# Kernel tuning notes

Measured on AMD Instinct MI355X. Metric: run time of the kernel, lower is better.

Reference implementation:

```python
import jax, jax.numpy as jnp
import numpy as np

NUM_HEADS = 4

def setup_inputs() -> dict:
    key = jax.random.key(0)
    ks = jax.random.split(key, 5)
    B, T, F, C = 2, 128, 256, 256
    # weights scaled ~1/sqrt(C) so softmax is not saturated
    s = 1.0 / np.sqrt(C)
    return {
        "x": jax.random.normal(ks[0], (B, T, F, C), jnp.float32),
        "w_in": jax.random.normal(ks[1], (3 * C, C), jnp.float32) * s,
        "b_in": jax.random.normal(ks[2], (3 * C,), jnp.float32) * 0.01,
        "w_out": jax.random.normal(ks[3], (C, C), jnp.float32) * s,
        "b_out": jax.random.normal(ks[4], (C,), jnp.float32) * 0.01,
        "band": 16,
    }

def reference(x, w_in, b_in, w_out, b_out, band):
    B, T, F, C = x.shape
    H = NUM_HEADS
    D = C // H
    x2 = x.reshape(B * T, F, C)  # attention over frequency, independent per (B,T)
    qkv = x2 @ w_in.T + b_in  # [BT, F, 3C]
    q, k, v = jnp.split(qkv, 3, axis=-1)
    def heads(t):
        return t.reshape(B * T, F, H, D).transpose(0, 2, 1, 3)  # [BT, H, F, D]
    q, k, v = heads(q), heads(k), heads(v)
    scores = jnp.einsum('bhid,bhjd->bhij', q, k) / jnp.sqrt(jnp.asarray(D, x.dtype))
    i = jnp.arange(F)[:, None]
    j = jnp.arange(F)[None, :]
    keep = jnp.abs(i - j) <= band  # banded locality mask [F, F]
    scores = jnp.where(keep, scores, -jnp.inf)
    attn = jax.nn.softmax(scores, axis=-1)
    out = jnp.einsum('bhij,bhjd->bhid', attn, v)  # [BT, H, F, D]
    out = out.transpose(0, 2, 1, 3).reshape(B * T, F, C)
    y = out @ w_out.T + b_out
    return y.reshape(B, T, F, C)
```

## Files before the change

### kernel.cpp

```cpp
#include <hip/hip_runtime.h>
#include <hip/hip_bf16.h>
#include <cstdint>

typedef unsigned int u32;
typedef __attribute__((ext_vector_type(8))) __bf16 bf16x8;
typedef __attribute__((ext_vector_type(4))) float f32x4;
typedef __attribute__((ext_vector_type(2))) _Float16 half2_t;
typedef __attribute__((ext_vector_type(4))) _Float16 half4;
typedef __attribute__((ext_vector_type(2))) __fp16 fp16x2;

#define BT_N 256
#define F_N 256
#define C_N 256
#define H_N 4
#define D_N 64
#define TC_N 768
#define M_N (BT_N * F_N)
#define VT_ST 268

__device__ __forceinline__ ushort f2bf(float f) {
  u32 u = __float_as_uint(f);
  u32 r = (u + 0x7fffu + ((u >> 16) & 1u)) >> 16;
  return (ushort)r;
}

__device__ __forceinline__ u32 pkbf(float a, float b) {
  return (u32)f2bf(a) | ((u32)f2bf(b) << 16);
}

__device__ __forceinline__ void gload_lds16(const ushort* g, ushort* l) {
  __builtin_amdgcn_global_load_lds(
      (const __attribute__((address_space(1))) u32*)g,
      (__attribute__((address_space(3))) u32*)l, 16, 0, 0);
}

#define WAITV(N) asm volatile("s_waitcnt vmcnt(" #N ")" ::: "memory")
#define BAR_IN  { __builtin_amdgcn_s_barrier(); \
                  asm volatile("" ::: "memory"); \
                  __builtin_amdgcn_sched_barrier(0); }
#define BAR_OUT { __builtin_amdgcn_sched_barrier(0); \
                  asm volatile("" ::: "memory"); \
                  __builtin_amdgcn_s_barrier(); }

__global__ __launch_bounds__(256) void cvt2_f32_bf16_k(
    const float* __restrict__ s0, ushort* __restrict__ d0, int n0,
    const float* __restrict__ s1, ushort* __restrict__ d1, int n1) {
  int idx = blockIdx.x * 256 + threadIdx.x;
  int stride = gridDim.x * 256;
  for (int i = idx; i < n0 + n1; i += stride) {
    const float4* s = (i < n0) ? ((const float4*)s0 + i) : ((const float4*)s1 + (i - n0));
    ushort* d = (i < n0) ? (d0 + (size_t)i * 4) : (d1 + (size_t)(i - n0) * 4);
    float4 v = *s;
    *(uint2*)d = make_uint2(pkbf(v.x, v.y), pkbf(v.z, v.w));
  }
}

__global__ __launch_bounds__(256) void gemm_qkv(
    const float* __restrict__ x, const ushort* __restrict__ wb,
    const float* __restrict__ bias, _Float16* __restrict__ qkv, int nwg8) {
  __shared__ ushort Bs[2][128 * 64];

  const int tid = threadIdx.x;
  const int lane = tid & 63;
  const int wid = tid >> 6;
  const int wr = wid >> 1, wc = wid & 1;
  const int l15 = lane & 15, g = lane >> 4;
  const int b = blockIdx.x;
  const int bid = (b & 7) * nwg8 + (b >> 3);
  const int rowBase = bid * 64;

  bf16x8 af[2][8];
#pragma unroll
  for (int i2 = 0; i2 < 2; ++i2) {
    const float* xr = x + (size_t)(rowBase + wr * 32 + i2 * 16 + l15) * 256 + g * 8;
#pragma unroll
    for (int ks = 0; ks < 8; ++ks) {
      float4 f0 = *(const float4*)(xr + ks * 32);
      float4 f1 = *(const float4*)(xr + ks * 32 + 4);
      uint4 pk = make_uint4(pkbf(f0.x, f0.y), pkbf(f0.z, f0.w),
                            pkbf(f1.x, f1.y), pkbf(f1.z, f1.w));
      af[i2][ks] = __builtin_bit_cast(bf16x8, pk);
    }
  }

  const int sr = tid >> 3;
  const int sc = tid & 7;
#define STAGE_B(buf, nt, kt)                                                  \
  {                                                                           \
    ushort* B_ = Bs[buf];                                                     \
    _Pragma("unroll") for (int p = 0; p < 4; ++p) {                           \
      int r = p * 32 + sr;                                                    \
      const ushort* gb = wb + (size_t)((nt) * 128 + r) * 256 + (kt) * 64 +    \
                         ((sc ^ (r & 7)) << 3);                               \
      gload_lds16(gb, B_ + (size_t)(p * 256 + tid) * 8);                      \
    }                                                                         \
  }

  f32x4 acc[2][4] = {};
  STAGE_B(0, 0, 0);

#pragma unroll
  for (int nt = 0; nt < 6; ++nt) {
#pragma unroll
    for (int kt = 0; kt < 4; ++kt) {
      const int s = nt * 4 + kt;
      if (s < 23) {
        const int nt2 = (s + 1) >> 2, kt2 = (s + 1) & 3;
        STAGE_B((s + 1) & 1, nt2, kt2);
        WAITV(4);
      } else {
        WAITV(0);
      }
      BAR_IN;
      const ushort* B_ = Bs[s & 1];
#pragma unroll
      for (int kk = 0; kk < 2; ++kk) {
        bf16x8 bfr[4];
#pragma unroll
        for (int j2 = 0; j2 < 4; ++j2) {
          int row = wc * 64 + j2 * 16 + l15;
          bfr[j2] = *(const bf16x8*)(B_ + row * 64 + (((kk * 4 + g) ^ (l15 & 7)) * 8));
        }
#pragma unroll
        for (int i2 = 0; i2 < 2; ++i2)
#pragma unroll
          for (int j2 = 0; j2 < 4; ++j2)
            acc[i2][j2] = __builtin_amdgcn_mfma_f32_16x16x32_bf16(
                bfr[j2], af[i2][kt * 2 + kk], acc[i2][j2], 0, 0, 0);
      }
      if (kt == 3) {
#pragma unroll
        for (int j2 = 0; j2 < 4; ++j2) {
          int col = nt * 128 + wc * 64 + j2 * 16 + g * 4;
          float4 bv = *(const float4*)(bias + col);
#pragma unroll
          for (int i2 = 0; i2 < 2; ++i2) {
            int row = rowBase + wr * 32 + i2 * 16 + l15;
            fp16x2 lo = __builtin_amdgcn_cvt_pkrtz(acc[i2][j2][0] + bv.x,
                                                   acc[i2][j2][1] + bv.y);
            fp16x2 hi = __builtin_amdgcn_cvt_pkrtz(acc[i2][j2][2] + bv.z,
                                                   acc[i2][j2][3] + bv.w);
            *(uint2*)(qkv + (size_t)row * 768 + col) =
                make_uint2(__builtin_bit_cast(u32, lo), __builtin_bit_cast(u32, hi));
            acc[i2][j2] = f32x4{0.f, 0.f, 0.f, 0.f};
          }
        }
      }
      BAR_OUT;
    }
  }
#undef STAGE_B
}

template <typename OutT>
__global__ __launch_bounds__(256, 2) void gemm_bt(
    const ushort* __restrict__ Ap, const ushort* __restrict__ Bp,
    const float* __restrict__ bias, OutT* __restrict__ Cp,
    int N, int NTN, int nwg8) {
  constexpr bool F32OUT = (sizeof(OutT) == 4);
  constexpr int SMEM_BYTES = F32OUT ? 67584 : 65536;
  __shared__ char smem[SMEM_BYTES];
  ushort* smemH = (ushort*)smem;

  const int tid = threadIdx.x;
  const int lane = tid & 63;
  const int wid = tid >> 6;
  const int wr = wid >> 1, wc = wid & 1;
  const int l15 = lane & 15, l4 = lane >> 4;
  const int b = blockIdx.x;
  const int bid = (b & 7) * nwg8 + (b >> 3);
  const int tm = bid / NTN;
  const int tn = bid - tm * NTN;
  const int rowBase = tm * 128, colBase = tn * 128;

  f32x4 acc[4][4] = {};

  const int ar = (tid >> 3);
  const int c8 = tid & 7;
  const int akk = ((c8 ^ (ar & 7)) << 3);
  const ushort* gB = Bp + (size_t)(colBase + ar) * 256 + akk;
  const ushort* gAh = Ap + (size_t)(rowBase + ar) * 256 + akk;

#define STAGE_AB(buf, k0)                                                     \
  {                                                                           \
    ushort* As_ = smemH + (buf) * 8192;                                       \
    ushort* Bs_ = smemH + 16384 + (buf) * 8192;                               \
    _Pragma("unroll") for (int c = 0; c < 4; ++c) {                           \
      gload_lds16(gAh + (size_t)(c * 32) * 256 + (k0),                        \
                  As_ + (size_t)(c * 256 + (wid << 6)) * 8);                  \
      gload_lds16(gB + (size_t)(c * 32) * 256 + (k0),                         \
                  Bs_ + (size_t)(c * 256 + (wid << 6)) * 8);                  \
    }                                                                         \
  }

  STAGE_AB(0, 0);

  int cur = 0;
#pragma unroll
  for (int t = 0; t < 4; ++t) {
    if (t < 3) {
      STAGE_AB(cur ^ 1, (t + 1) * 64);
      WAITV(8);
    } else {
      WAITV(0);
    }
    BAR_IN;
    const ushort* As_ = smemH + cur * 8192;
    const ushort* Bs_ = smemH + 16384 + cur * 8192;
#pragma unroll
    for (int kk = 0; kk < 2; ++kk) {
      bf16x8 af[4];
      bf16x8 bfr[4];
#pragma unroll
      for (int i2 = 0; i2 < 4; ++i2) {
        int row = wr * 64 + i2 * 16 + l15;
        af[i2] = *(const bf16x8*)(As_ + row * 64 + (((kk * 4 + l4) ^ (l15 & 7)) * 8));
      }
#pragma unroll
      for (int j2 = 0; j2 < 4; ++j2) {
        int row = wc * 64 + j2 * 16 + l15;
        bfr[j2] = *(const bf16x8*)(Bs_ + row * 64 + (((kk * 4 + l4) ^ (l15 & 7)) * 8));
      }
#pragma unroll
      for (int i2 = 0; i2 < 4; ++i2)
#pragma unroll
        for (int j2 = 0; j2 < 4; ++j2)
          acc[i2][j2] = __builtin_amdgcn_mfma_f32_16x16x32_bf16(
              af[i2], bfr[j2], acc[i2][j2], 0, 0, 0);
    }
    BAR_OUT;
    cur ^= 1;
  }
#undef STAGE_AB

  __syncthreads();
  if constexpr (F32OUT) {
    float* eb = (float*)smem;
#pragma unroll
    for (int j2 = 0; j2 < 4; ++j2) {
      float bv = bias[colBase + wc * 64 + j2 * 16 + l15];
#pragma unroll
      for (int i2 = 0; i2 < 4; ++i2)
#pragma unroll
        for (int r = 0; r < 4; ++r)
          eb[(wr * 64 + i2 * 16 + l4 * 4 + r) * 132 + wc * 64 + j2 * 16 + l15] =
              acc[i2][j2][r] + bv;
    }
    __syncthreads();
#pragma unroll
    for (int i = 0; i < 32; ++i) {
      int row = wid * 32 + i;
      uint2 d = *(const uint2*)((const u32*)eb + row * 132 + lane * 2);
      *(uint2*)((float*)Cp + (size_t)(rowBase + row) * N + colBase + lane * 2) = d;
    }
  } else {
    ushort* eb = smemH;
#pragma unroll
    for (int j2 = 0; j2 < 4; ++j2) {
      float bv = bias[colBase + wc * 64 + j2 * 16 + l15];
#pragma unroll
      for (int i2 = 0; i2 < 4; ++i2)
#pragma unroll
        for (int r = 0; r < 4; ++r) {
          _Float16 h = (_Float16)(acc[i2][j2][r] + bv);
          eb[(wr * 64 + i2 * 16 + l4 * 4 + r) * 136 + wc * 64 + j2 * 16 + l15] =
              __builtin_bit_cast(ushort, h);
        }
    }
    __syncthreads();
#pragma unroll
    for (int i = 0; i < 16; ++i) {
      int row = wid * 32 + 2 * i + (lane >> 5);
      int hl = lane & 31;
      uint2 d = *(const uint2*)(eb + row * 136 + hl * 4);
      *(uint2*)((_Float16*)Cp + (size_t)(rowBase + row) * N + colBase + hl * 4) = d;
    }
  }
}

__global__ __launch_bounds__(256) void attn_mfma(
    const _Float16* __restrict__ qkv, ushort* __restrict__ aout) {
  __shared__ ushort smem[18432 + 64 * VT_ST];
  const int tid = threadIdx.x;
  const int bt = blockIdx.x >> 2;
  const int h = blockIdx.x & 3;
  const _Float16* base = qkv + (size_t)bt * 256 * 768 + h * 64;
  ushort* klds = smem;
  ushort* vlds = smem + 18432;

  {
    const int r0 = tid >> 3, c8 = tid & 7;
#pragma unroll
    for (int p = 0; p < 8; ++p) {
      int j = p * 32 + r0;
      const uint4 k4 = *(const uint4*)(base + (size_t)j * 768 + 256 + c8 * 8);
      *(uint4*)(klds + j * 72 + c8 * 8) = k4;
      const uint4 v4 = *(const uint4*)(base + (size_t)j * 768 + 512 + c8 * 8);
      const ushort* vh = (const ushort*)&v4;
      ushort* vtp = vlds + (c8 * 8) * VT_ST + j;
#pragma unroll
      for (int i = 0; i < 8; ++i) vtp[i * VT_ST] = vh[i];
    }
  }

  const int w = tid >> 6, lane = tid & 63;
  const int l15 = lane & 15, g = lane >> 4, g4 = g * 4;

  uint2 qf0[4], qf1[4], qf2[4], qf3[4];
  {
    const uint2* q0 = (const uint2*)(base + (size_t)(w * 64 + 0 * 16 + l15) * 768 + g4);
    const uint2* q1 = (const uint2*)(base + (size_t)(w * 64 + 1 * 16 + l15) * 768 + g4);
    const uint2* q2 = (const uint2*)(base + (size_t)(w * 64 + 2 * 16 + l15) * 768 + g4);
    const uint2* q3 = (const uint2*)(base + (size_t)(w * 64 + 3 * 16 + l15) * 768 + g4);
#pragma unroll
    for (int ks = 0; ks < 4; ++ks) {
      qf0[ks] = q0[ks * 4]; qf1[ks] = q1[ks * 4];
      qf2[ks] = q2[ks * 4]; qf3[ks] = q3[ks * 4];
    }
  }

  u32 bb = 0;
#pragma unroll
  for (int jt = 0; jt < 3; ++jt)
#pragma unroll
    for (int r = 0; r < 4; ++r) {
      int d = 16 * jt + g4 + r - 16 - l15;
      if (d >= -16 && d <= 16) bb |= 1u << (jt * 4 + r);
    }

  __syncthreads();

  const float SC = 0.18033688f;

#pragma unroll
  for (int rt = 0; rt < 4; ++rt) {
    const int R0 = w * 64 + rt * 16;
    const int Jc = R0 - 16;
    const uint2* qf = (rt == 0) ? qf0 : (rt == 1) ? qf1 : (rt == 2) ? qf2 : qf3;

    f32x4 st[3] = {};
#pragma unroll
    for (int jt = 0; jt < 3; ++jt) {
      int krow = Jc + 16 * jt + l15;
      krow = krow < 0 ? 0 : (krow > 255 ? 255 : krow);
      const ushort* kp = klds + krow * 72 + g4;
#pragma unroll
      for (int ks = 0; ks < 4; ++ks) {
        uint2 kf = *(const uint2*)(kp + ks * 16);
        st[jt] = __builtin_amdgcn_mfma_f32_16x16x16f16(
            __builtin_bit_cast(half4, kf), __builtin_bit_cast(half4, qf[ks]),
            st[jt], 0, 0, 0);
      }
    }

    float l_acc = 0.f;
    float pp[3][4];
#pragma unroll
    for (int jt = 0; jt < 3; ++jt)
#pragma unroll
      for (int r = 0; r < 4; ++r) {
        int jg = Jc + 16 * jt + g4 + r;
        bool keep = (((bb >> (jt * 4 + r)) & 1u) != 0) && (jg >= 0) && (jg < 256);
        float pv = keep ? __builtin_amdgcn_exp2f(st[jt][r] * SC) : 0.f;
        pp[jt][r] = pv;
        l_acc += pv;
      }
    l_acc += __shfl_xor(l_acc, 16, 64);
    l_acc += __shfl_xor(l_acc, 32, 64);
    const float inv = 1.f / l_acc;

    uint2 pf[3];
#pragma unroll
    for (int jt = 0; jt < 3; ++jt) {
      fp16x2 a = __builtin_amdgcn_cvt_pkrtz(pp[jt][0] * inv, pp[jt][1] * inv);
      fp16x2 c = __builtin_amdgcn_cvt_pkrtz(pp[jt][2] * inv, pp[jt][3] * inv);
      pf[jt].x = __builtin_bit_cast(u32, a);
      pf[jt].y = __builtin_bit_cast(u32, c);
    }

    f32x4 ot[4] = {};
#pragma unroll
    for (int kt = 0; kt < 3; ++kt) {
      int jb = Jc + 16 * kt + g4;
      jb = jb < 0 ? 0 : (jb > 252 ? 252 : jb);
#pragma unroll
      for (int mt = 0; mt < 4; ++mt) {
        uint2 vfr = *(const uint2*)(vlds + (16 * mt + l15) * VT_ST + jb);
        ot[mt] = __builtin_amdgcn_mfma_f32_16x16x16f16(
            __builtin_bit_cast(half4, vfr), __builtin_bit_cast(half4, pf[kt]),
            ot[mt], 0, 0, 0);
      }
    }

    ushort* orow = aout + (size_t)(bt * 256 + R0 + l15) * 256 + h * 64 + g4;
#pragma unroll
    for (int mt = 0; mt < 4; ++mt) {
      u32 lo = (u32)f2bf(ot[mt][0]) | ((u32)f2bf(ot[mt][1]) << 16);
      u32 hi = (u32)f2bf(ot[mt][2]) | ((u32)f2bf(ot[mt][3]) << 16);
      *(uint2*)(orow + mt * 16) = make_uint2(lo, hi);
    }
  }
}

extern "C" void kernel_launch(void* const* d_in, const int* in_sizes, int n_in,
                              void* d_out, int out_size, void* d_ws, size_t ws_size,
                              hipStream_t stream) {
  const float* x = (const float*)d_in[0];
  const float* w_in = (const float*)d_in[1];
  const float* b_in = (const float*)d_in[2];
  const float* w_out = (const float*)d_in[3];
  const float* b_out = (const float*)d_in[4];
  float* y = (float*)d_out;

  char* ws = (char*)d_ws;
  const size_t qkv_bytes = (size_t)M_N * TC_N * 2;
  _Float16* qkv = (_Float16*)ws;
  ushort* attn = (ushort*)(ws + qkv_bytes);
  ushort* winb = attn + (size_t)M_N * C_N;
  ushort* woutb = winb + TC_N * C_N;

  cvt2_f32_bf16_k<<<256, 256, 0, stream>>>(w_in, winb, TC_N * C_N / 4,
                                           w_out, woutb, C_N * C_N / 4);

  gemm_qkv<<<M_N / 64, 256, 0, stream>>>(x, winb, b_in, qkv, (M_N / 64) / 8);

  attn_mfma<<<BT_N * H_N, 256, 0, stream>>>(qkv, attn);

  gemm_bt<float><<<(M_N / 128) * (C_N / 128), 256, 0, stream>>>(
      attn, woutb, b_out, y, C_N, C_N / 128, (M_N / 128) * (C_N / 128) / 8);
}
```

Baseline: 111.4 us.

## Restructure QKV GEMM into 128x128 tiles with fp32 A staged via LDS

Replaces the QKV projection kernel, which held one 64-row A block in registers and swept all 768 columns. The new kernel uses 128x128 output tiles with double-buffered LDS for both operands. A is loaded as fp32, converted to bf16 in registers, and written to swizzled LDS, while B uses direct global-to-LDS loads. The epilogue stages fp16 results through LDS so stores are coalesced. The intent is better MFMA utilization and store efficiency, at the cost of re-reading the fp32 input once per column tile.

```diff
diff --git a/kernel.cpp b/kernel.cpp
--- a/kernel.cpp
+++ b/kernel.cpp
@@ -35,6 +35,9 @@
 }
 
 #define WAITV(N) asm volatile("s_waitcnt vmcnt(" #N ")" ::: "memory")
+#define BARX { asm volatile("s_waitcnt lgkmcnt(0)" ::: "memory"); \
+               __builtin_amdgcn_s_barrier(); \
+               __builtin_amdgcn_sched_barrier(0); }
 #define BAR_IN  { __builtin_amdgcn_s_barrier(); \
                   asm volatile("" ::: "memory"); \
                   __builtin_amdgcn_sched_barrier(0); }
@@ -55,111 +58,11 @@
   }
 }
 
-__global__ __launch_bounds__(256) void gemm_qkv(
-    const float* __restrict__ x, const ushort* __restrict__ wb,
-    const float* __restrict__ bias, _Float16* __restrict__ qkv, int nwg8) {
-  __shared__ ushort Bs[2][128 * 64];
-
-  const int tid = threadIdx.x;
-  const int lane = tid & 63;
-  const int wid = tid >> 6;
-  const int wr = wid >> 1, wc = wid & 1;
-  const int l15 = lane & 15, g = lane >> 4;
-  const int b = blockIdx.x;
-  const int bid = (b & 7) * nwg8 + (b >> 3);
-  const int rowBase = bid * 64;
-
-  bf16x8 af[2][8];
-#pragma unroll
-  for (int i2 = 0; i2 < 2; ++i2) {
-    const float* xr = x + (size_t)(rowBase + wr * 32 + i2 * 16 + l15) * 256 + g * 8;
-#pragma unroll
-    for (int ks = 0; ks < 8; ++ks) {
-      float4 f0 = *(const float4*)(xr + ks * 32);
-      float4 f1 = *(const float4*)(xr + ks * 32 + 4);
-      uint4 pk = make_uint4(pkbf(f0.x, f0.y), pkbf(f0.z, f0.w),
-                            pkbf(f1.x, f1.y), pkbf(f1.z, f1.w));
-      af[i2][ks] = __builtin_bit_cast(bf16x8, pk);
-    }
-  }
-
-  const int sr = tid >> 3;
-  const int sc = tid & 7;
-#define STAGE_B(buf, nt, kt)                                                  \
-  {                                                                           \
-    ushort* B_ = Bs[buf];                                                     \
-    _Pragma("unroll") for (int p = 0; p < 4; ++p) {                           \
-      int r = p * 32 + sr;                                                    \
-      const ushort* gb = wb + (size_t)((nt) * 128 + r) * 256 + (kt) * 64 +    \
-                         ((sc ^ (r & 7)) << 3);                               \
-      gload_lds16(gb, B_ + (size_t)(p * 256 + tid) * 8);                      \
-    }                                                                         \
-  }
-
-  f32x4 acc[2][4] = {};
-  STAGE_B(0, 0, 0);
-
-#pragma unroll
-  for (int nt = 0; nt < 6; ++nt) {
-#pragma unroll
-    for (int kt = 0; kt < 4; ++kt) {
-      const int s = nt * 4 + kt;
-      if (s < 23) {
-        const int nt2 = (s + 1) >> 2, kt2 = (s + 1) & 3;
-        STAGE_B((s + 1) & 1, nt2, kt2);
-        WAITV(4);
-      } else {
-        WAITV(0);
-      }
-      BAR_IN;
-      const ushort* B_ = Bs[s & 1];
-#pragma unroll
-      for (int kk = 0; kk < 2; ++kk) {
-        bf16x8 bfr[4];
-#pragma unroll
-        for (int j2 = 0; j2 < 4; ++j2) {
-          int row = wc * 64 + j2 * 16 + l15;
-          bfr[j2] = *(const bf16x8*)(B_ + row * 64 + (((kk * 4 + g) ^ (l15 & 7)) * 8));
-        }
-#pragma unroll
-        for (int i2 = 0; i2 < 2; ++i2)
-#pragma unroll
-          for (int j2 = 0; j2 < 4; ++j2)
-            acc[i2][j2] = __builtin_amdgcn_mfma_f32_16x16x32_bf16(
-                bfr[j2], af[i2][kt * 2 + kk], acc[i2][j2], 0, 0, 0);
-      }
-      if (kt == 3) {
-#pragma unroll
-        for (int j2 = 0; j2 < 4; ++j2) {
-          int col = nt * 128 + wc * 64 + j2 * 16 + g * 4;
-          float4 bv = *(const float4*)(bias + col);
-#pragma unroll
-          for (int i2 = 0; i2 < 2; ++i2) {
-            int row = rowBase + wr * 32 + i2 * 16 + l15;
-            fp16x2 lo = __builtin_amdgcn_cvt_pkrtz(acc[i2][j2][0] + bv.x,
-                                                   acc[i2][j2][1] + bv.y);
-            fp16x2 hi = __builtin_amdgcn_cvt_pkrtz(acc[i2][j2][2] + bv.z,
-                                                   acc[i2][j2][3] + bv.w);
-            *(uint2*)(qkv + (size_t)row * 768 + col) =
-                make_uint2(__builtin_bit_cast(u32, lo), __builtin_bit_cast(u32, hi));
-            acc[i2][j2] = f32x4{0.f, 0.f, 0.f, 0.f};
-          }
-        }
-      }
-      BAR_OUT;
-    }
-  }
-#undef STAGE_B
-}
-
-template <typename OutT>
-__global__ __launch_bounds__(256, 2) void gemm_bt(
-    const ushort* __restrict__ Ap, const ushort* __restrict__ Bp,
-    const float* __restrict__ bias, OutT* __restrict__ Cp,
-    int N, int NTN, int nwg8) {
-  constexpr bool F32OUT = (sizeof(OutT) == 4);
-  constexpr int SMEM_BYTES = F32OUT ? 67584 : 65536;
-  __shared__ char smem[SMEM_BYTES];
+__global__ __launch_bounds__(256, 2) void gemm_qkv_f32(
+    const float* __restrict__ x, const ushort* __restrict__ Bp,
+    const float* __restrict__ bias, _Float16* __restrict__ Cp,
+    int NTN, int nwg8) {
+  __shared__ char smem[65536];
   ushort* smemH = (ushort*)smem;
 
   const int tid = threadIdx.x;
@@ -179,6 +82,132 @@
   const int c8 = tid & 7;
   const int akk = ((c8 ^ (ar & 7)) << 3);
   const ushort* gB = Bp + (size_t)(colBase + ar) * 256 + akk;
+  const float* gA = x + (size_t)(rowBase + ar) * 256 + akk;
+
+  float4 rA[2][4][2];
+
+#define LOAD_AF(rb, k0)                                                       \
+  {                                                                           \
+    _Pragma("unroll") for (int c = 0; c < 4; ++c) {                           \
+      const float* ga = gA + (size_t)(c * 32) * 256 + (k0);                   \
+      rA[rb][c][0] = *(const float4*)ga;                                      \
+      rA[rb][c][1] = *(const float4*)(ga + 4);                                \
+    }                                                                         \
+  }
+#define WRITE_AF(lb, rb)                                                      \
+  {                                                                           \
+    ushort* As_ = smemH + (lb) * 8192;                                        \
+    _Pragma("unroll") for (int c = 0; c < 4; ++c) {                           \
+      uint4 pk = make_uint4(pkbf(rA[rb][c][0].x, rA[rb][c][0].y),             \
+                            pkbf(rA[rb][c][0].z, rA[rb][c][0].w),             \
+                            pkbf(rA[rb][c][1].x, rA[rb][c][1].y),             \
+                            pkbf(rA[rb][c][1].z, rA[rb][c][1].w));            \
+      *(uint4*)(As_ + (ar + 32 * c) * 64 + c8 * 8) = pk;                      \
+    }                                                                         \
+  }
+#define STAGE_B(lb, k0)                                                       \
+  {                                                                           \
+    ushort* Bs_ = smemH + 16384 + (lb) * 8192;                                \
+    _Pragma("unroll") for (int c = 0; c < 4; ++c)                             \
+      gload_lds16(gB + (size_t)(c * 32) * 256 + (k0),                         \
+                  Bs_ + (size_t)(c * 256 + (wid << 6)) * 8);                  \
+  }
+
+  LOAD_AF(0, 0);
+  STAGE_B(0, 0);
+  LOAD_AF(1, 64);
+  WAITV(12);
+  WRITE_AF(0, 0);
+
+#pragma unroll
+  for (int t = 0; t < 4; ++t) {
+    if (t < 3) STAGE_B((t + 1) & 1, (t + 1) * 64);
+    if (t < 2) LOAD_AF(t & 1, (t + 2) * 64);
+    if (t < 2) { WAITV(12); } else if (t == 2) { WAITV(4); } else { WAITV(0); }
+    BARX;
+    const ushort* As_ = smemH + (t & 1) * 8192;
+    const ushort* Bs_ = smemH + 16384 + (t & 1) * 8192;
+#pragma unroll
+    for (int kk = 0; kk < 2; ++kk) {
+      bf16x8 af[4];
+      bf16x8 bfr[4];
+#pragma unroll
+      for (int i2 = 0; i2 < 4; ++i2) {
+        int row = wr * 64 + i2 * 16 + l15;
+        af[i2] = *(const bf16x8*)(As_ + row * 64 + (((kk * 4 + l4) ^ (l15 & 7)) * 8));
+      }
+#pragma unroll
+      for (int j2 = 0; j2 < 4; ++j2) {
+        int row = wc * 64 + j2 * 16 + l15;
+        bfr[j2] = *(const bf16x8*)(Bs_ + row * 64 + (((kk * 4 + l4) ^ (l15 & 7)) * 8));
+      }
+#pragma unroll
+      for (int i2 = 0; i2 < 4; ++i2)
+#pragma unroll
+        for (int j2 = 0; j2 < 4; ++j2)
+          acc[i2][j2] = __builtin_amdgcn_mfma_f32_16x16x32_bf16(
+              af[i2], bfr[j2], acc[i2][j2], 0, 0, 0);
+    }
+    if (t < 3) WRITE_AF((t + 1) & 1, (t + 1) & 1);
+    BARX;
+  }
+#undef LOAD_AF
+#undef WRITE_AF
+#undef STAGE_B
+
+  __syncthreads();
+  {
+    ushort* eb = smemH;
+#pragma unroll
+    for (int j2 = 0; j2 < 4; ++j2) {
+      float bv = bias[colBase + wc * 64 + j2 * 16 + l15];
+#pragma unroll
+      for (int i2 = 0; i2 < 4; ++i2)
+#pragma unroll
+        for (int r = 0; r < 4; ++r) {
+          _Float16 h = (_Float16)(acc[i2][j2][r] + bv);
+          eb[(wr * 64 + i2 * 16 + l4 * 4 + r) * 136 + wc * 64 + j2 * 16 + l15] =
+              __builtin_bit_cast(ushort, h);
+        }
+    }
+    __syncthreads();
+#pragma unroll
+    for (int i = 0; i < 16; ++i) {
+      int row = wid * 32 + 2 * i + (lane >> 5);
+      int hl = lane & 31;
+      uint2 d = *(const uint2*)(eb + row * 136 + hl * 4);
+      *(uint2*)((_Float16*)Cp + (size_t)(rowBase + row) * TC_N + colBase + hl * 4) = d;
+    }
+  }
+}
+
+template <typename OutT>
+__global__ __launch_bounds__(256, 2) void gemm_bt(
+    const ushort* __restrict__ Ap, const ushort* __restrict__ Bp,
+    const float* __restrict__ bias, OutT* __restrict__ Cp,
+    int N, int NTN, int nwg8) {
+  constexpr bool F32OUT = (sizeof(OutT) == 4);
+  constexpr int SMEM_BYTES = F32OUT ? 67584 : 65536;
+  __shared__ char smem[SMEM_BYTES];
+  ushort* smemH = (ushort*)smem;
+
+  const int tid = threadIdx.x;
+  const int lane = tid & 63;
+  const int wid = tid >> 6;
+  const int wr = wid >> 1, wc = wid & 1;
+  const int l15 = lane & 15, l4 = lane >> 4;
+  const int b = blockIdx.x;
+  const int bid = (b & 7) * nwg8 + (b >> 3);
+  const int tm = bid / NTN;
+  const int tn = bid - tm * NTN;
+  const int rowBase = tm * 128, colBase = tn * 128;
+
+  f32x4 acc[4][4] = {};
+
+  const int ar = (tid >> 3);
+  const int c8 = tid & 7;
+  const int akk = ((c8 ^ (ar & 7)) << 3);
+  const ushort* gB = Bp + (size_t)(colBase + ar) * 256 + akk;
   const ushort* gAh = Ap + (size_t)(rowBase + ar) * 256 + akk;
 
 #define STAGE_AB(buf, k0)                                                     \
@@ -422,7 +451,8 @@
   cvt2_f32_bf16_k<<<256, 256, 0, stream>>>(w_in, winb, TC_N * C_N / 4,
                                            w_out, woutb, C_N * C_N / 4);
 
-  gemm_qkv<<<M_N / 64, 256, 0, stream>>>(x, winb, b_in, qkv, (M_N / 64) / 8);
+  gemm_qkv_f32<<<(M_N / 128) * (TC_N / 128), 256, 0, stream>>>(
+      x, winb, b_in, qkv, TC_N / 128, (M_N / 128) * (TC_N / 128) / 8);
 
   attn_mfma<<<BT_N * H_N, 256, 0, stream>>>(qkv, attn);
 
```

Result: no change. 113.2 us (+1.6%).
